# Performance work log

Measured on AMD Instinct MI355X. Metric: run time of the kernel, lower is better.

Reference implementation:

```python
import jax, jax.numpy as jnp
import numpy as np

N = 50000      # nodes
E = 800000     # edges (before self loops)
IN, H, OUT = 128, 64, 64
NEG_SLOPE = 0.2  # PyG GATConv leaky_relu slope


def _glorot(k, shape):
    lim = float(np.sqrt(6.0 / (shape[0] + shape[1])))
    return jax.random.uniform(k, shape, jnp.float32, -lim, lim)


def setup_inputs() -> dict:
    key = jax.random.key(0)
    ks = jax.random.split(key, 16)
    x = jax.random.normal(ks[0], (N, IN), jnp.float32)
    edge_src = jax.random.randint(ks[1], (E,), 0, N, jnp.int32)
    edge_dst = jax.random.randint(ks[2], (E,), 0, N, jnp.int32)
    dims = [(IN, H), (H, H), (H, OUT)]
    inp = {"x": x, "edge_src": edge_src, "edge_dst": edge_dst}
    i = 3
    for l, (di, do) in enumerate(dims):
        inp[f"W{l}"] = _glorot(ks[i], (di, do)); i += 1
        inp[f"as{l}"] = _glorot(ks[i], (1, do))[0]; i += 1
        inp[f"ad{l}"] = _glorot(ks[i], (1, do))[0]; i += 1
        inp[f"b{l}"] = jnp.zeros((do,), jnp.float32)
    return inp


def _gat_layer(x, W, a_src, a_dst, b, src, dst):
    # single-head GATConv (PyG semantics, self loops already in src/dst)
    h = x @ W                              # [N, do]
    s = h @ a_src                          # [N] source attention logits
    d = h @ a_dst                          # [N] dest attention logits
    e = jax.nn.leaky_relu(s[src] + d[dst], NEG_SLOPE)   # [E']
    # segment softmax over incoming edges of each destination node
    m = jax.ops.segment_max(e, dst, num_segments=N)
    w = jnp.exp(e - m[dst])
    denom = jax.ops.segment_sum(w, dst, num_segments=N)
    coef = w / (denom[dst] + 1e-16)
    out = jax.ops.segment_sum(h[src] * coef[:, None], dst, num_segments=N)
    return out + b


def reference(x, edge_src, edge_dst, W0, as0, ad0, b0, W1, as1, ad1, b1, W2, as2, ad2, b2):
    # add self loops (GATConv default add_self_loops=True)
    loop = jnp.arange(N, dtype=edge_src.dtype)
    src = jnp.concatenate([edge_src, loop])
    dst = jnp.concatenate([edge_dst, loop])
    h = jax.nn.relu(_gat_layer(x, W0, as0, ad0, b0, src, dst))
    # dropout is identity in eval mode
    h = jax.nn.relu(_gat_layer(h, W1, as1, ad1, b1, src, dst))
    return _gat_layer(h, W2, as2, ad2, b2, src, dst)
```

## Files before the change

kernel.cpp:

```cpp
#include <hip/hip_runtime.h>
#include <hip/hip_fp16.h>
#include <math.h>

#define WAVE 64
#define NEG_SLOPE 0.2f
#define LSTR 68

typedef _Float16 half8 __attribute__((ext_vector_type(8)));
typedef float f32x4 __attribute__((ext_vector_type(4)));


__global__ __launch_bounds__(256) void bucket_count_kernel(
    const int* __restrict__ dst, int* __restrict__ gcnt, int e, int nb) {
    extern __shared__ int cnt[];
    for (int b = threadIdx.x; b < nb; b += 256) cnt[b] = 0;
    __syncthreads();
    int base = blockIdx.x * 4096;
#pragma unroll
    for (int k = 0; k < 16; ++k) {
        int i = base + k * 256 + threadIdx.x;
        if (i < e) atomicAdd(&cnt[dst[i] >> 7], 1);
    }
    __syncthreads();
    for (int b = threadIdx.x; b < nb; b += 256) {
        int c = cnt[b];
        if (c) atomicAdd(&gcnt[b], c);
    }
}

__global__ __launch_bounds__(512) void bucket_scan_kernel(
    const int* __restrict__ gcnt, int* __restrict__ boff, int* __restrict__ gfill,
    int* __restrict__ rowptr, int nb, int e, int n) {
    __shared__ int sh[512];
    int t = threadIdx.x;
    int v = (t < nb) ? gcnt[t] : 0;
    sh[t] = v;
    __syncthreads();
    for (int o = 1; o < 512; o <<= 1) {
        int u = (t >= o) ? sh[t - o] : 0;
        __syncthreads();
        sh[t] += u;
        __syncthreads();
    }
    if (t < nb) { int ex = sh[t] - v; boff[t] = ex; gfill[t] = ex; }
    if (t == 0) { boff[nb] = e; rowptr[n] = e + n; }
}

__global__ __launch_bounds__(256) void bucket_place_kernel(
    const int* __restrict__ src, const int* __restrict__ dst,
    int* __restrict__ gfill, int* __restrict__ binned, int e, int nb) {
    extern __shared__ int lds[];
    int* cnt = lds;
    int* bas = lds + nb;
    for (int b = threadIdx.x; b < nb; b += 256) cnt[b] = 0;
    __syncthreads();
    int base = blockIdx.x * 4096;
#pragma unroll
    for (int k = 0; k < 16; ++k) {
        int i = base + k * 256 + threadIdx.x;
        if (i < e) atomicAdd(&cnt[dst[i] >> 7], 1);
    }
    __syncthreads();
    for (int b = threadIdx.x; b < nb; b += 256) {
        int c = cnt[b];
        bas[b] = c ? atomicAdd(&gfill[b], c) : 0;
        cnt[b] = 0;
    }
    __syncthreads();
#pragma unroll
    for (int k = 0; k < 16; ++k) {
        int i = base + k * 256 + threadIdx.x;
        if (i < e) {
            int d = dst[i];
            int bk = d >> 7;
            int r = atomicAdd(&cnt[bk], 1);
            binned[bas[bk] + r] = ((d & 127) << 16) | src[i];
        }
    }
}

__global__ __launch_bounds__(256) void bucket_build_kernel(
    const int* __restrict__ binned, const int* __restrict__ boff,
    int* __restrict__ csr_src, int* __restrict__ rowptr, int n) {
    __shared__ int cnt[128], off[128], pcnt[128];
    int b = blockIdx.x;
    int t = threadIdx.x;
    int nodeBase = b << 7;
    int nc = min(128, n - nodeBase);
    int e0 = boff[b], e1 = boff[b + 1];
    int ne = e1 - e0;
    if (t < 128) { cnt[t] = 1; pcnt[t] = 1; }
    __syncthreads();
    for (int i = t; i < ne; i += 256)
        atomicAdd(&cnt[binned[e0 + i] >> 16], 1);
    __syncthreads();
    if (t < 128) off[t] = cnt[t];
    __syncthreads();
    for (int o = 1; o < 128; o <<= 1) {
        int u = (t >= o && t < 128) ? off[t - o] : 0;
        __syncthreads();
        if (t < 128) off[t] += u;
        __syncthreads();
    }
    if (t < 128) off[t] -= cnt[t];
    __syncthreads();
    int csrBase = e0 + nodeBase;
    if (t < nc) {
        rowptr[nodeBase + t] = csrBase + off[t];
        csr_src[csrBase + off[t]] = nodeBase + t;
    }
    for (int i = t; i < ne; i += 256) {
        int p = binned[e0 + i];
        int loc = p >> 16;
        int r = atomicAdd(&pcnt[loc], 1);
        csr_src[csrBase + off[loc] + r] = p & 0xFFFF;
    }
}


template <int K>
__global__ __launch_bounds__(256) void mfma_gemm_feat_kernel(
    const float* __restrict__ X, const float* __restrict__ W,
    const float* __restrict__ a_s, const float* __restrict__ a_d,
    __half* __restrict__ H, float* __restrict__ S, float* __restrict__ D, int n) {
    constexpr int AK = K + 8;
    __shared__ _Float16 Xs[64 * AK];
    __shared__ _Float16 Bt[64 * AK];
    int t = threadIdx.x;
    int base = blockIdx.x * 64;

    {
        int row = t >> 2, q = t & 3;
        int grow = base + row;
        constexpr int CW = K / 4;
#pragma unroll
        for (int c0 = 0; c0 < CW; c0 += 8) {
            float4 v0 = make_float4(0.f, 0.f, 0.f, 0.f), v1 = v0;
            if (grow < n) {
                v0 = *(const float4*)(X + (size_t)grow * K + q * CW + c0);
                v1 = *(const float4*)(X + (size_t)grow * K + q * CW + c0 + 4);
            }
            _Float16 h[8] = {(_Float16)v0.x, (_Float16)v0.y, (_Float16)v0.z, (_Float16)v0.w,
                             (_Float16)v1.x, (_Float16)v1.y, (_Float16)v1.z, (_Float16)v1.w};
            *(uint4*)(Xs + row * AK + q * CW + c0) = *(uint4*)h;
        }
    }
    {
        int nn = t & 63, g = t >> 6;
        constexpr int KW = K / 4;
        _Float16 hbuf[KW];
#pragma unroll
        for (int j = 0; j < KW; ++j)
            hbuf[j] = (_Float16)W[(size_t)(g * KW + j) * 64 + nn];
#pragma unroll
        for (int j = 0; j < KW; j += 8)
            *(uint4*)(Bt + nn * AK + g * KW + j) = *(uint4*)(hbuf + j);
    }
    __syncthreads();

    int lane = t & 63;
    int wv = t >> 6;
    int m0 = wv * 16;
    int l15 = lane & 15, quad = lane >> 4;

    f32x4 acc[4] = {{0.f, 0.f, 0.f, 0.f}, {0.f, 0.f, 0.f, 0.f},
                    {0.f, 0.f, 0.f, 0.f}, {0.f, 0.f, 0.f, 0.f}};
#pragma unroll
    for (int ks = 0; ks < K; ks += 32) {
        half8 a = *(half8*)(Xs + (m0 + l15) * AK + ks + quad * 8);
#pragma unroll
        for (int cg = 0; cg < 4; ++cg) {
            half8 b = *(half8*)(Bt + (cg * 16 + l15) * AK + ks + quad * 8);
            acc[cg] = __builtin_amdgcn_mfma_f32_16x16x32_f16(a, b, acc[cg], 0, 0, 0);
        }
    }

    float as_c[4], ad_c[4];
#pragma unroll
    for (int cg = 0; cg < 4; ++cg) {
        as_c[cg] = a_s[cg * 16 + l15];
        ad_c[cg] = a_d[cg * 16 + l15];
    }
#pragma unroll
    for (int r = 0; r < 4; ++r) {
        int grow = base + m0 + quad * 4 + r;
        bool ok = grow < n;
        float ps = 0.f, pd = 0.f;
#pragma unroll
        for (int cg = 0; cg < 4; ++cg) {
            float v = acc[cg][r];
            if (ok) H[(size_t)grow * 64 + cg * 16 + l15] = __float2half(v);
            ps += v * as_c[cg];
            pd += v * ad_c[cg];
        }
        for (int o = 1; o < 16; o <<= 1) {
            ps += __shfl_xor(ps, o);
            pd += __shfl_xor(pd, o);
        }
        if (l15 == 0 && ok) { S[grow] = ps; D[grow] = pd; }
    }
}


__global__ __launch_bounds__(256) void gat_aggregate_kernel(
    const __half* __restrict__ H, const float* __restrict__ S,
    const float* __restrict__ D, const int* __restrict__ rowptr,
    const int* __restrict__ csr_src, const float* __restrict__ bias,
    float* __restrict__ OUT, int n, int do_relu) {
    int wid  = (blockIdx.x * blockDim.x + threadIdx.x) >> 6;
    int lane = threadIdx.x & 63;
    if (wid >= n) return;
    int eg = lane >> 3;
    int cg = lane & 7;
    int start = rowptr[wid];
    int end   = rowptr[wid + 1];
    float d_i = D[wid];

    float z = 0.f;
    float acc[8] = {0.f, 0.f, 0.f, 0.f, 0.f, 0.f, 0.f, 0.f};

    for (int cb = start; cb < end; cb += WAVE) {
        int j = cb + lane;
        bool v = j < end;
        int sc = v ? csr_src[j] : 0;
        float sv = S[sc];
        float e = sv + d_i;
        e = (e > 0.f) ? e : NEG_SLOPE * e;
        float w = v ? __expf(e) : 0.f;
        z += w;

        int nch = min(WAVE, end - cb);
        int rounds = (nch + 7) >> 3;
#pragma unroll 4
        for (int r = 0; r < rounds; ++r) {
            int idx = 8 * r + eg;
            float wr = __shfl(w, idx);
            int   sr = __shfl(sc, idx);
            if (idx < nch) {
                uint4 u = *(const uint4*)(H + (size_t)sr * 64 + 8 * cg);
                float2 f0 = __half22float2(*(__half2*)&u.x);
                float2 f1 = __half22float2(*(__half2*)&u.y);
                float2 f2 = __half22float2(*(__half2*)&u.z);
                float2 f3 = __half22float2(*(__half2*)&u.w);
                acc[0] = fmaf(wr, f0.x, acc[0]);
                acc[1] = fmaf(wr, f0.y, acc[1]);
                acc[2] = fmaf(wr, f1.x, acc[2]);
                acc[3] = fmaf(wr, f1.y, acc[3]);
                acc[4] = fmaf(wr, f2.x, acc[4]);
                acc[5] = fmaf(wr, f2.y, acc[5]);
                acc[6] = fmaf(wr, f3.x, acc[6]);
                acc[7] = fmaf(wr, f3.y, acc[7]);
            }
        }
    }

    z += __shfl_xor(z, 1);
    z += __shfl_xor(z, 2);
    z += __shfl_xor(z, 4);
    for (int o = 8; o < 64; o <<= 1) {
#pragma unroll
        for (int jj = 0; jj < 8; ++jj) acc[jj] += __shfl_xor(acc[jj], o);
        z += __shfl_xor(z, o);
    }

    if (eg == 0) {
        float inv = 1.f / (z + 1e-16f);
        const float4 bv0 = *(const float4*)(bias + 8 * cg);
        const float4 bv1 = *(const float4*)(bias + 8 * cg + 4);
        float4 o0, o1;
        o0.x = acc[0] * inv + bv0.x;
        o0.y = acc[1] * inv + bv0.y;
        o0.z = acc[2] * inv + bv0.z;
        o0.w = acc[3] * inv + bv0.w;
        o1.x = acc[4] * inv + bv1.x;
        o1.y = acc[5] * inv + bv1.y;
        o1.z = acc[6] * inv + bv1.z;
        o1.w = acc[7] * inv + bv1.w;
        if (do_relu) {
            o0.x = fmaxf(o0.x, 0.f); o0.y = fmaxf(o0.y, 0.f);
            o0.z = fmaxf(o0.z, 0.f); o0.w = fmaxf(o0.w, 0.f);
            o1.x = fmaxf(o1.x, 0.f); o1.y = fmaxf(o1.y, 0.f);
            o1.z = fmaxf(o1.z, 0.f); o1.w = fmaxf(o1.w, 0.f);
        }
        *(float4*)(OUT + (size_t)wid * 64 + 8 * cg) = o0;
        *(float4*)(OUT + (size_t)wid * 64 + 8 * cg + 4) = o1;
    }
}


static inline size_t align256(size_t x) { return (x + 255) & ~(size_t)255; }

extern "C" void kernel_launch(void* const* d_in, const int* in_sizes, int n_in,
                              void* d_out, int out_size, void* d_ws, size_t ws_size,
                              hipStream_t stream) {
    const float* x    = (const float*)d_in[0];
    const int*   esrc = (const int*)d_in[1];
    const int*   edst = (const int*)d_in[2];
    const int E = in_sizes[1];
    const int N = in_sizes[0] / 128;

    const float* W0 = (const float*)d_in[3];
    const float* as0 = (const float*)d_in[4];
    const float* ad0 = (const float*)d_in[5];
    const float* b0 = (const float*)d_in[6];
    const float* W1 = (const float*)d_in[7];
    const float* as1 = (const float*)d_in[8];
    const float* ad1 = (const float*)d_in[9];
    const float* b1 = (const float*)d_in[10];
    const float* W2 = (const float*)d_in[11];
    const float* as2 = (const float*)d_in[12];
    const float* ad2 = (const float*)d_in[13];
    const float* b2 = (const float*)d_in[14];

    const int NB = (N + 127) >> 7;

    char* p = (char*)d_ws;
    int* gcnt    = (int*)p; p += align256((size_t)(NB + 1) * 4);
    int* boff    = (int*)p; p += align256((size_t)(NB + 1) * 4);
    int* gfill   = (int*)p; p += align256((size_t)(NB + 1) * 4);
    int* rowptr  = (int*)p; p += align256((size_t)(N + 1) * 4);
    int* csr_src = (int*)p; p += align256((size_t)(E + N) * 4);
    int* binned  = (int*)p; p += align256((size_t)E * 4);
    __half* h16 = (__half*)p; p += align256((size_t)N * 64 * 2);
    float* sA = (float*)p; p += align256((size_t)N * 4);
    float* dA = (float*)p; p += align256((size_t)N * 4);
    float* XA = (float*)p; p += align256((size_t)N * 64 * 4);
    float* XB = (float*)p; p += align256((size_t)N * 64 * 4);
    float* out = (float*)d_out;

    int nchunk = (E + 4095) / 4096;
    hipMemsetAsync(gcnt, 0, (size_t)(NB + 1) * 4, stream);
    bucket_count_kernel<<<nchunk, 256, NB * 4, stream>>>(edst, gcnt, E, NB);
    bucket_scan_kernel<<<1, 512, 0, stream>>>(gcnt, boff, gfill, rowptr, NB, E, N);
    bucket_place_kernel<<<nchunk, 256, 2 * NB * 4, stream>>>(esrc, edst, gfill, binned, E, NB);
    bucket_build_kernel<<<NB, 256, 0, stream>>>(binned, boff, csr_src, rowptr, N);

    int tile_grid = (N + 63) / 64;
    int agg_grid  = (N + 3) / 4;

    mfma_gemm_feat_kernel<128><<<tile_grid, 256, 0, stream>>>(x, W0, as0, ad0, h16, sA, dA, N);
    gat_aggregate_kernel<<<agg_grid, 256, 0, stream>>>(h16, sA, dA, rowptr, csr_src, b0, XA, N, 1);

    mfma_gemm_feat_kernel<64><<<tile_grid, 256, 0, stream>>>(XA, W1, as1, ad1, h16, sA, dA, N);
    gat_aggregate_kernel<<<agg_grid, 256, 0, stream>>>(h16, sA, dA, rowptr, csr_src, b1, XB, N, 1);

    mfma_gemm_feat_kernel<64><<<tile_grid, 256, 0, stream>>>(XB, W2, as2, ad2, h16, sA, dA, N);
    gat_aggregate_kernel<<<agg_grid, 256, 0, stream>>>(h16, sA, dA, rowptr, csr_src, b2, out, N, 0);
}
```

Baseline: 252.2 us.

## Fuse edge binning with first GEMM, use fixed-capacity buckets and fp16 activations

Removes the bucket count and scan passes by placing edges into fixed-capacity per-bucket slots, and runs the edge placement in the same launch as the layer-0 feature GEMM. The CSR now stores start/end pairs per node in padded per-bucket regions. Intermediate layer outputs are stored as fp16, and later GEMMs read them directly. This cuts launches and halves activation traffic, but edges beyond the 4096-per-bucket capacity would be dropped silently, and storing activations in fp16 adds rounding error.

Result: faster. 235.0 us (-6.8%).

```diff
diff --git a/kernel.cpp b/kernel.cpp
--- a/kernel.cpp
+++ b/kernel.cpp
@@ -4,54 +4,122 @@
 
 #define WAVE 64
 #define NEG_SLOPE 0.2f
-#define LSTR 68
+#define BCAP 4096
+#define CSTR (BCAP + 128)
 
 typedef _Float16 half8 __attribute__((ext_vector_type(8)));
 typedef float f32x4 __attribute__((ext_vector_type(4)));
 
 
-__global__ __launch_bounds__(256) void bucket_count_kernel(
-    const int* __restrict__ dst, int* __restrict__ gcnt, int e, int nb) {
-    extern __shared__ int cnt[];
-    for (int b = threadIdx.x; b < nb; b += 256) cnt[b] = 0;
-    __syncthreads();
-    int base = blockIdx.x * 4096;
-#pragma unroll
-    for (int k = 0; k < 16; ++k) {
-        int i = base + k * 256 + threadIdx.x;
-        if (i < e) atomicAdd(&cnt[dst[i] >> 7], 1);
-    }
-    __syncthreads();
-    for (int b = threadIdx.x; b < nb; b += 256) {
-        int c = cnt[b];
-        if (c) atomicAdd(&gcnt[b], c);
-    }
-}
-
-__global__ __launch_bounds__(512) void bucket_scan_kernel(
-    const int* __restrict__ gcnt, int* __restrict__ boff, int* __restrict__ gfill,
-    int* __restrict__ rowptr, int nb, int e, int n) {
-    __shared__ int sh[512];
-    int t = threadIdx.x;
-    int v = (t < nb) ? gcnt[t] : 0;
-    sh[t] = v;
-    __syncthreads();
-    for (int o = 1; o < 512; o <<= 1) {
-        int u = (t >= o) ? sh[t - o] : 0;
-        __syncthreads();
-        sh[t] += u;
-        __syncthreads();
-    }
-    if (t < nb) { int ex = sh[t] - v; boff[t] = ex; gfill[t] = ex; }
-    if (t == 0) { boff[nb] = e; rowptr[n] = e + n; }
-}
-
-__global__ __launch_bounds__(256) void bucket_place_kernel(
+template <int K, int IS_HALF>
+__device__ __forceinline__ void gemm_body(
+    char* smemRaw, int t, int bid,
+    const void* __restrict__ Xv, const float* __restrict__ W,
+    const float* __restrict__ a_s, const float* __restrict__ a_d,
+    __half* __restrict__ H, float* __restrict__ S, float* __restrict__ D,
+    int n) {
+    constexpr int AK = K + 8;
+    _Float16* Xs = (_Float16*)smemRaw;
+    _Float16* Bt = Xs + 64 * AK;
+    int base = bid * 64;
+
+    {
+        int row = t >> 2, q = t & 3;
+        int grow = base + row;
+        constexpr int CW = K / 4;
+        if constexpr (IS_HALF) {
+            const __half* Xh = (const __half*)Xv;
+#pragma unroll
+            for (int c0 = 0; c0 < CW; c0 += 8) {
+                uint4 v = make_uint4(0, 0, 0, 0);
+                if (grow < n) v = *(const uint4*)(Xh + (size_t)grow * K + q * CW + c0);
+                *(uint4*)(Xs + row * AK + q * CW + c0) = v;
+            }
+        } else {
+            const float* X = (const float*)Xv;
+#pragma unroll
+            for (int c0 = 0; c0 < CW; c0 += 8) {
+                float4 v0 = make_float4(0.f, 0.f, 0.f, 0.f), v1 = v0;
+                if (grow < n) {
+                    v0 = *(const float4*)(X + (size_t)grow * K + q * CW + c0);
+                    v1 = *(const float4*)(X + (size_t)grow * K + q * CW + c0 + 4);
+                }
+                _Float16 h[8] = {(_Float16)v0.x, (_Float16)v0.y, (_Float16)v0.z, (_Float16)v0.w,
+                                 (_Float16)v1.x, (_Float16)v1.y, (_Float16)v1.z, (_Float16)v1.w};
+                *(uint4*)(Xs + row * AK + q * CW + c0) = *(uint4*)h;
+            }
+        }
+    }
+    {
+        int nn = t & 63, g = t >> 6;
+        constexpr int KW = K / 4;
+        _Float16 hbuf[KW];
+#pragma unroll
+        for (int j = 0; j < KW; ++j)
+            hbuf[j] = (_Float16)W[(size_t)(g * KW + j) * 64 + nn];
+#pragma unroll
+        for (int j = 0; j < KW; j += 8)
+            *(uint4*)(Bt + nn * AK + g * KW + j) = *(uint4*)(hbuf + j);
+    }
+    __syncthreads();
+
+    int lane = t & 63;
+    int wv = t >> 6;
+    int m0 = wv * 16;
+    int l15 = lane & 15, quad = lane >> 4;
+
+    f32x4 acc[4] = {{0.f, 0.f, 0.f, 0.f}, {0.f, 0.f, 0.f, 0.f},
+                    {0.f, 0.f, 0.f, 0.f}, {0.f, 0.f, 0.f, 0.f}};
+#pragma unroll
+    for (int ks = 0; ks < K; ks += 32) {
+        half8 a = *(half8*)(Xs + (m0 + l15) * AK + ks + quad * 8);
+#pragma unroll
+        for (int cg = 0; cg < 4; ++cg) {
+            half8 b = *(half8*)(Bt + (cg * 16 + l15) * AK + ks + quad * 8);
+            acc[cg] = __builtin_amdgcn_mfma_f32_16x16x32_f16(a, b, acc[cg], 0, 0, 0);
+        }
+    }
+
+    float as_c[4], ad_c[4];
+#pragma unroll
+    for (int cg = 0; cg < 4; ++cg) {
+        as_c[cg] = a_s[cg * 16 + l15];
+        ad_c[cg] = a_d[cg * 16 + l15];
+    }
+#pragma unroll
+    for (int r = 0; r < 4; ++r) {
+        int grow = base + m0 + quad * 4 + r;
+        bool ok = grow < n;
+        float ps = 0.f, pd = 0.f;
+#pragma unroll
+        for (int cg = 0; cg < 4; ++cg) {
+            float v = acc[cg][r];
+            if (ok) H[(size_t)grow * 64 + cg * 16 + l15] = __float2half(v);
+            ps += v * as_c[cg];
+            pd += v * ad_c[cg];
+        }
+        for (int o = 1; o < 16; o <<= 1) {
+            ps += __shfl_xor(ps, o);
+            pd += __shfl_xor(pd, o);
+        }
+        if (l15 == 0 && ok) { S[grow] = ps; D[grow] = pd; }
+    }
+}
+
+__global__ __launch_bounds__(256) void place_gemm0_kernel(
     const int* __restrict__ src, const int* __restrict__ dst,
-    int* __restrict__ gfill, int* __restrict__ binned, int e, int nb) {
-    extern __shared__ int lds[];
-    int* cnt = lds;
-    int* bas = lds + nb;
+    int* __restrict__ gfill, int* __restrict__ binned, int e, int nb, int nchunk,
+    const float* __restrict__ X, const float* __restrict__ W,
+    const float* __restrict__ a_s, const float* __restrict__ a_d,
+    __half* __restrict__ H, float* __restrict__ S, float* __restrict__ D, int n) {
+    extern __shared__ char smem[];
+    if ((int)blockIdx.x >= nchunk) {
+        gemm_body<128, 0>(smem, threadIdx.x, blockIdx.x - nchunk,
+                          X, W, a_s, a_d, H, S, D, n);
+        return;
+    }
+    int* cnt = (int*)smem;
+    int* bas = cnt + nb;
     for (int b = threadIdx.x; b < nb; b += 256) cnt[b] = 0;
     __syncthreads();
     int base = blockIdx.x * 4096;
@@ -74,25 +142,25 @@
             int d = dst[i];
             int bk = d >> 7;
             int r = atomicAdd(&cnt[bk], 1);
-            binned[bas[bk] + r] = ((d & 127) << 16) | src[i];
+            binned[(size_t)bk * BCAP + bas[bk] + r] = ((d & 127) << 16) | src[i];
         }
     }
 }
 
 __global__ __launch_bounds__(256) void bucket_build_kernel(
-    const int* __restrict__ binned, const int* __restrict__ boff,
-    int* __restrict__ csr_src, int* __restrict__ rowptr, int n) {
+    const int* __restrict__ binned, const int* __restrict__ gfill,
+    int* __restrict__ csr_src, int2* __restrict__ rowse, int n) {
     __shared__ int cnt[128], off[128], pcnt[128];
     int b = blockIdx.x;
     int t = threadIdx.x;
     int nodeBase = b << 7;
     int nc = min(128, n - nodeBase);
-    int e0 = boff[b], e1 = boff[b + 1];
-    int ne = e1 - e0;
+    int ne = min(gfill[b], BCAP);
+    const int* bp = binned + (size_t)b * BCAP;
     if (t < 128) { cnt[t] = 1; pcnt[t] = 1; }
     __syncthreads();
     for (int i = t; i < ne; i += 256)
-        atomicAdd(&cnt[binned[e0 + i] >> 16], 1);
+        atomicAdd(&cnt[bp[i] >> 16], 1);
     __syncthreads();
     if (t < 128) off[t] = cnt[t];
     __syncthreads();
@@ -104,116 +172,43 @@
     }
     if (t < 128) off[t] -= cnt[t];
     __syncthreads();
-    int csrBase = e0 + nodeBase;
+    int csrBase = b * CSTR;
     if (t < nc) {
-        rowptr[nodeBase + t] = csrBase + off[t];
-        csr_src[csrBase + off[t]] = nodeBase + t;
+        int st = csrBase + off[t];
+        rowse[nodeBase + t] = make_int2(st, st + cnt[t]);
+        csr_src[st] = nodeBase + t;
     }
     for (int i = t; i < ne; i += 256) {
-        int p = binned[e0 + i];
+        int p = bp[i];
         int loc = p >> 16;
         int r = atomicAdd(&pcnt[loc], 1);
         csr_src[csrBase + off[loc] + r] = p & 0xFFFF;
     }
 }
 
-
-template <int K>
+template <int K, int IS_HALF>
 __global__ __launch_bounds__(256) void mfma_gemm_feat_kernel(
-    const float* __restrict__ X, const float* __restrict__ W,
+    const void* __restrict__ Xv, const float* __restrict__ W,
     const float* __restrict__ a_s, const float* __restrict__ a_d,
     __half* __restrict__ H, float* __restrict__ S, float* __restrict__ D, int n) {
-    constexpr int AK = K + 8;
-    __shared__ _Float16 Xs[64 * AK];
-    __shared__ _Float16 Bt[64 * AK];
-    int t = threadIdx.x;
-    int base = blockIdx.x * 64;
-
-    {
-        int row = t >> 2, q = t & 3;
-        int grow = base + row;
-        constexpr int CW = K / 4;
-#pragma unroll
-        for (int c0 = 0; c0 < CW; c0 += 8) {
-            float4 v0 = make_float4(0.f, 0.f, 0.f, 0.f), v1 = v0;
-            if (grow < n) {
-                v0 = *(const float4*)(X + (size_t)grow * K + q * CW + c0);
-                v1 = *(const float4*)(X + (size_t)grow * K + q * CW + c0 + 4);
-            }
-            _Float16 h[8] = {(_Float16)v0.x, (_Float16)v0.y, (_Float16)v0.z, (_Float16)v0.w,
-                             (_Float16)v1.x, (_Float16)v1.y, (_Float16)v1.z, (_Float16)v1.w};
-            *(uint4*)(Xs + row * AK + q * CW + c0) = *(uint4*)h;
-        }
-    }
-    {
-        int nn = t & 63, g = t >> 6;
-        constexpr int KW = K / 4;
-        _Float16 hbuf[KW];
-#pragma unroll
-        for (int j = 0; j < KW; ++j)
-            hbuf[j] = (_Float16)W[(size_t)(g * KW + j) * 64 + nn];
-#pragma unroll
-        for (int j = 0; j < KW; j += 8)
-            *(uint4*)(Bt + nn * AK + g * KW + j) = *(uint4*)(hbuf + j);
-    }
-    __syncthreads();
-
-    int lane = t & 63;
-    int wv = t >> 6;
-    int m0 = wv * 16;
-    int l15 = lane & 15, quad = lane >> 4;
-
-    f32x4 acc[4] = {{0.f, 0.f, 0.f, 0.f}, {0.f, 0.f, 0.f, 0.f},
-                    {0.f, 0.f, 0.f, 0.f}, {0.f, 0.f, 0.f, 0.f}};
-#pragma unroll
-    for (int ks = 0; ks < K; ks += 32) {
-        half8 a = *(half8*)(Xs + (m0 + l15) * AK + ks + quad * 8);
-#pragma unroll
-        for (int cg = 0; cg < 4; ++cg) {
-            half8 b = *(half8*)(Bt + (cg * 16 + l15) * AK + ks + quad * 8);
-            acc[cg] = __builtin_amdgcn_mfma_f32_16x16x32_f16(a, b, acc[cg], 0, 0, 0);
-        }
-    }
-
-    float as_c[4], ad_c[4];
-#pragma unroll
-    for (int cg = 0; cg < 4; ++cg) {
-        as_c[cg] = a_s[cg * 16 + l15];
-        ad_c[cg] = a_d[cg * 16 + l15];
-    }
-#pragma unroll
-    for (int r = 0; r < 4; ++r) {
-        int grow = base + m0 + quad * 4 + r;
-        bool ok = grow < n;
-        float ps = 0.f, pd = 0.f;
-#pragma unroll
-        for (int cg = 0; cg < 4; ++cg) {
-            float v = acc[cg][r];
-            if (ok) H[(size_t)grow * 64 + cg * 16 + l15] = __float2half(v);
-            ps += v * as_c[cg];
-            pd += v * ad_c[cg];
-        }
-        for (int o = 1; o < 16; o <<= 1) {
-            ps += __shfl_xor(ps, o);
-            pd += __shfl_xor(pd, o);
-        }
-        if (l15 == 0 && ok) { S[grow] = ps; D[grow] = pd; }
-    }
-}
-
-
+    __shared__ char smem[2 * 64 * (K + 8) * 2];
+    gemm_body<K, IS_HALF>(smem, threadIdx.x, blockIdx.x, Xv, W, a_s, a_d, H, S, D, n);
+}
+
+
+template <int WRITE_HALF>
 __global__ __launch_bounds__(256) void gat_aggregate_kernel(
     const __half* __restrict__ H, const float* __restrict__ S,
-    const float* __restrict__ D, const int* __restrict__ rowptr,
+    const float* __restrict__ D, const int2* __restrict__ rowse,
     const int* __restrict__ csr_src, const float* __restrict__ bias,
-    float* __restrict__ OUT, int n, int do_relu) {
+    void* __restrict__ OUTp, int n, int do_relu) {
     int wid  = (blockIdx.x * blockDim.x + threadIdx.x) >> 6;
     int lane = threadIdx.x & 63;
     if (wid >= n) return;
     int eg = lane >> 3;
     int cg = lane & 7;
-    int start = rowptr[wid];
-    int end   = rowptr[wid + 1];
+    int2 se = rowse[wid];
+    int start = se.x, end = se.y;
     float d_i = D[wid];
 
     float z = 0.f;
@@ -267,23 +262,29 @@
         float inv = 1.f / (z + 1e-16f);
         const float4 bv0 = *(const float4*)(bias + 8 * cg);
         const float4 bv1 = *(const float4*)(bias + 8 * cg + 4);
-        float4 o0, o1;
-        o0.x = acc[0] * inv + bv0.x;
-        o0.y = acc[1] * inv + bv0.y;
-        o0.z = acc[2] * inv + bv0.z;
-        o0.w = acc[3] * inv + bv0.w;
-        o1.x = acc[4] * inv + bv1.x;
-        o1.y = acc[5] * inv + bv1.y;
-        o1.z = acc[6] * inv + bv1.z;
-        o1.w = acc[7] * inv + bv1.w;
+        float o[8];
+        o[0] = acc[0] * inv + bv0.x;
+        o[1] = acc[1] * inv + bv0.y;
+        o[2] = acc[2] * inv + bv0.z;
+        o[3] = acc[3] * inv + bv0.w;
+        o[4] = acc[4] * inv + bv1.x;
+        o[5] = acc[5] * inv + bv1.y;
+        o[6] = acc[6] * inv + bv1.z;
+        o[7] = acc[7] * inv + bv1.w;
         if (do_relu) {
-            o0.x = fmaxf(o0.x, 0.f); o0.y = fmaxf(o0.y, 0.f);
-            o0.z = fmaxf(o0.z, 0.f); o0.w = fmaxf(o0.w, 0.f);
-            o1.x = fmaxf(o1.x, 0.f); o1.y = fmaxf(o1.y, 0.f);
-            o1.z = fmaxf(o1.z, 0.f); o1.w = fmaxf(o1.w, 0.f);
-        }
-        *(float4*)(OUT + (size_t)wid * 64 + 8 * cg) = o0;
-        *(float4*)(OUT + (size_t)wid * 64 + 8 * cg + 4) = o1;
+#pragma unroll
+            for (int jj = 0; jj < 8; ++jj) o[jj] = fmaxf(o[jj], 0.f);
+        }
+        if constexpr (WRITE_HALF) {
+            _Float16 h[8];
+#pragma unroll
+            for (int jj = 0; jj < 8; ++jj) h[jj] = (_Float16)o[jj];
+            *(uint4*)((__half*)OUTp + (size_t)wid * 64 + 8 * cg) = *(uint4*)h;
+        } else {
+            float* OUT = (float*)OUTp;
+            *(float4*)(OUT + (size_t)wid * 64 + 8 * cg) = make_float4(o[0], o[1], o[2], o[3]);
+            *(float4*)(OUT + (size_t)wid * 64 + 8 * cg + 4) = make_float4(o[4], o[5], o[6], o[7]);
+        }
     }
 }
 
@@ -315,35 +316,37 @@
     const int NB = (N + 127) >> 7;
 
     char* p = (char*)d_ws;
-    int* gcnt    = (int*)p; p += align256((size_t)(NB + 1) * 4);
-    int* boff    = (int*)p; p += align256((size_t)(NB + 1) * 4);
-    int* gfill   = (int*)p; p += align256((size_t)(NB + 1) * 4);
-    int* rowptr  = (int*)p; p += align256((size_t)(N + 1) * 4);
-    int* csr_src = (int*)p; p += align256((size_t)(E + N) * 4);
-    int* binned  = (int*)p; p += align256((size_t)E * 4);
+    int*  gfill   = (int*)p;  p += align256((size_t)(NB + 1) * 4);
+    int2* rowse   = (int2*)p; p += align256((size_t)N * 8);
+    int*  csr_src = (int*)p;  p += align256((size_t)NB * CSTR * 4);
+    int*  binned  = (int*)p;  p += align256((size_t)NB * BCAP * 4);
     __half* h16 = (__half*)p; p += align256((size_t)N * 64 * 2);
+    __half* hA  = (__half*)p; p += align256((size_t)N * 64 * 2);
+    __half* hB  = (__half*)p; p += align256((size_t)N * 64 * 2);
     float* sA = (float*)p; p += align256((size_t)N * 4);
     float* dA = (float*)p; p += align256((size_t)N * 4);
-    float* XA = (float*)p; p += align256((size_t)N * 64 * 4);
-    float* XB = (float*)p; p += align256((size_t)N * 64 * 4);
     float* out = (float*)d_out;
 
     int nchunk = (E + 4095) / 4096;
-    hipMemsetAsync(gcnt, 0, (size_t)(NB + 1) * 4, stream);
-    bucket_count_kernel<<<nchunk, 256, NB * 4, stream>>>(edst, gcnt, E, NB);
-    bucket_scan_kernel<<<1, 512, 0, stream>>>(gcnt, boff, gfill, rowptr, NB, E, N);
-    bucket_place_kernel<<<nchunk, 256, 2 * NB * 4, stream>>>(esrc, edst, gfill, binned, E, NB);
-    bucket_build_kernel<<<NB, 256, 0, stream>>>(binned, boff, csr_src, rowptr, N);
-
     int tile_grid = (N + 63) / 64;
     int agg_grid  = (N + 3) / 4;
 
-    mfma_gemm_feat_kernel<128><<<tile_grid, 256, 0, stream>>>(x, W0, as0, ad0, h16, sA, dA, N);
-    gat_aggregate_kernel<<<agg_grid, 256, 0, stream>>>(h16, sA, dA, rowptr, csr_src, b0, XA, N, 1);
-
-    mfma_gemm_feat_kernel<64><<<tile_grid, 256, 0, stream>>>(XA, W1, as1, ad1, h16, sA, dA, N);
-    gat_aggregate_kernel<<<agg_grid, 256, 0, stream>>>(h16, sA, dA, rowptr, csr_src, b1, XB, N, 1);
-
-    mfma_gemm_feat_kernel<64><<<tile_grid, 256, 0, stream>>>(XB, W2, as2, ad2, h16, sA, dA, N);
-    gat_aggregate_kernel<<<agg_grid, 256, 0, stream>>>(h16, sA, dA, rowptr, csr_src, b2, out, N, 0);
-}
+    hipMemsetAsync(gfill, 0, (size_t)(NB + 1) * 4, stream);
+
+    place_gemm0_kernel<<<nchunk + tile_grid, 256, 34816, stream>>>(
+        esrc, edst, gfill, binned, E, NB, nchunk,
+        x, W0, as0, ad0, h16, sA, dA, N);
+
+    bucket_build_kernel<<<NB, 256, 0, stream>>>(binned, gfill, csr_src, rowse, N);
+
+    gat_aggregate_kernel<1><<<agg_grid, 256, 0, stream>>>(
+        h16, sA, dA, rowse, csr_src, b0, hA, N, 1);
+
+    mfma_gemm_feat_kernel<64, 1><<<tile_grid, 256, 0, stream>>>(hA, W1, as1, ad1, h16, sA, dA, N);
+    gat_aggregate_kernel<1><<<agg_grid, 256, 0, stream>>>(
+        h16, sA, dA, rowse, csr_src, b1, hB, N, 1);
+
+    mfma_gemm_feat_kernel<64, 1><<<tile_grid, 256, 0, stream>>>(hB, W2, as2, ad2, h16, sA, dA, N);
+    gat_aggregate_kernel<0><<<agg_grid, 256, 0, stream>>>(
+        h16, sA, dA, rowse, csr_src, b2, out, N, 0);
+}
```
